# Kernel optimization log

Hardware: AMD Instinct MI355X
Metric: run time of the kernel (lower is better)

The kernel has to match this reference:

```python
import jax, jax.numpy as jnp
import numpy as np

N = 50000          # nodes (cells)
G = 1000           # input genes
E = 800000         # edges
HIDDEN = 128
HEADS = 8
C_HID = HIDDEN // HEADS   # 16 per-head channels
LATENT = 16
NEG_SLOPE = 0.2


def _gat_layer(x, src, dst, W, a_src, a_dst, b, heads, out_ch, concat):
    """PyG GATConv (shared lin for src/dst, add_self_loops=False, eval mode)."""
    n = x.shape[0]
    h = (x @ W).reshape(n, heads, out_ch)                 # [N,H,C]
    al_s = jnp.einsum('nhc,hc->nh', h, a_src)             # [N,H]
    al_d = jnp.einsum('nhc,hc->nh', h, a_dst)             # [N,H]
    logits = jax.nn.leaky_relu(al_s[src] + al_d[dst], NEG_SLOPE)  # [E,H]
    # segment softmax over destination neighborhoods
    m = jax.ops.segment_max(logits, dst, num_segments=n)  # [N,H]
    m = jnp.where(jnp.isfinite(m), m, 0.0)                # empty segments -> 0
    e = jnp.exp(logits - m[dst])                          # [E,H]
    denom = jax.ops.segment_sum(e, dst, num_segments=n)   # [N,H]
    alpha = e / (denom[dst] + 1e-16)                      # [E,H]
    msg = h[src] * alpha[:, :, None]                      # [E,H,C]
    out = jax.ops.segment_sum(msg, dst, num_segments=n)   # [N,H,C]
    out = out.reshape(n, heads * out_ch) if concat else out.mean(axis=1)
    return out + b


def setup_inputs() -> dict:
    key = jax.random.key(0)
    ks = jax.random.split(key, 16)
    x = jax.random.normal(ks[0], (N, G), dtype=jnp.float32)
    edge_index = jax.random.randint(ks[1], (2, E), 0, N, dtype=jnp.int64)

    def glorot(k, shape):
        fan_in, fan_out = shape[0], shape[-1]
        s = jnp.sqrt(6.0 / (fan_in + fan_out)).astype(jnp.float32)
        return jax.random.uniform(k, shape, jnp.float32, -s, s)

    # layer 0: G -> 8 heads x 16 (concat -> 128)
    W0 = glorot(ks[2], (G, HEADS * C_HID))
    as0 = glorot(ks[3], (HEADS, C_HID))
    ad0 = glorot(ks[4], (HEADS, C_HID))
    b0 = jnp.zeros((HEADS * C_HID,), jnp.float32)
    # layer 1: 128 -> 8 heads x 16 (concat -> 128)
    W1 = glorot(ks[5], (HIDDEN, HEADS * C_HID))
    as1 = glorot(ks[6], (HEADS, C_HID))
    ad1 = glorot(ks[7], (HEADS, C_HID))
    b1 = jnp.zeros((HEADS * C_HID,), jnp.float32)
    # layer 2: 128 -> 1 head x 16 (concat=False -> 16)
    W2 = glorot(ks[8], (HIDDEN, LATENT))
    as2 = glorot(ks[9], (1, LATENT))
    ad2 = glorot(ks[10], (1, LATENT))
    b2 = jnp.zeros((LATENT,), jnp.float32)

    return {"x": x, "edge_index": edge_index,
            "W0": W0, "as0": as0, "ad0": ad0, "b0": b0,
            "W1": W1, "as1": as1, "ad1": ad1, "b1": b1,
            "W2": W2, "as2": as2, "ad2": ad2, "b2": b2}


def reference(x, edge_index, W0, as0, ad0, b0, W1, as1, ad1, b1, W2, as2, ad2, b2):
    src, dst = edge_index[0], edge_index[1]
    h = _gat_layer(x, src, dst, W0, as0, ad0, b0, HEADS, C_HID, concat=True)
    h = jax.nn.elu(h)
    h = _gat_layer(h, src, dst, W1, as1, ad1, b1, HEADS, C_HID, concat=True)
    h = jax.nn.elu(h)
    z = _gat_layer(h, src, dst, W2, as2, ad2, b2, 1, LATENT, concat=False)
    return z
```

## Files before the change

### kernel.cpp

```cpp
#include <hip/hip_runtime.h>
#include <hip/hip_bf16.h>
#include <math.h>

#define GENES 1000

typedef __attribute__((ext_vector_type(8))) _Float16 half8;
typedef __attribute__((ext_vector_type(4))) float f32x4;
typedef __attribute__((ext_vector_type(4))) unsigned int uint4v;
typedef __attribute__((ext_vector_type(2))) unsigned int uint2v;

__device__ inline float f16lo(unsigned int v) {
  return (float)__builtin_bit_cast(_Float16, (unsigned short)(v & 0xffffu));
}
__device__ inline float f16hi(unsigned int v) {
  return (float)__builtin_bit_cast(_Float16, (unsigned short)(v >> 16));
}


__global__ void k_deg(const int* __restrict__ ei, int* __restrict__ deg, int E) {
  int e = blockIdx.x * blockDim.x + threadIdx.x;
  if (e < E) atomicAdd(&deg[ei[E + e]], 1);
}

__global__ void k_scan1(const int* __restrict__ deg, int* __restrict__ ptr,
                        int* __restrict__ bsum, int n) {
  __shared__ int ws[4];
  int t = threadIdx.x, b = blockIdx.x;
  int i = b * 256 + t;
  int lane = t & 63, w = t >> 6;
  int x = (i < n) ? deg[i] : 0;
  #pragma unroll
  for (int d = 1; d < 64; d <<= 1) {
    int y = __shfl_up(x, d);
    if (lane >= d) x += y;
  }
  if (lane == 63) ws[w] = x;
  __syncthreads();
  if (t == 0) {
    int s = 0;
    #pragma unroll
    for (int k = 0; k < 4; ++k) { s += ws[k]; ws[k] = s; }
  }
  __syncthreads();
  int incl = x + (w ? ws[w - 1] : 0);
  if (i < n) ptr[i + 1] = incl;
  if (t == 255) bsum[b] = incl;
  if (i == 0) ptr[0] = 0;
}

__global__ void k_scan2(int* __restrict__ bsum, int nb) {
  __shared__ int ws[4];
  int t = threadIdx.x;
  int lane = t & 63, w = t >> 6;
  int v = (t < nb) ? bsum[t] : 0;
  int x = v;
  #pragma unroll
  for (int d = 1; d < 64; d <<= 1) {
    int y = __shfl_up(x, d);
    if (lane >= d) x += y;
  }
  if (lane == 63) ws[w] = x;
  __syncthreads();
  if (t == 0) {
    int s = 0;
    #pragma unroll
    for (int k = 0; k < 4; ++k) { s += ws[k]; ws[k] = s; }
  }
  __syncthreads();
  int incl = x + (w ? ws[w - 1] : 0);
  if (t < nb) bsum[t] = incl - v;
}

__global__ void k_scan3(int* __restrict__ ptr, const int* __restrict__ bsum, int n) {
  int i = blockIdx.x * 256 + threadIdx.x;
  if (i < n) ptr[i + 1] += bsum[blockIdx.x];
}

__global__ void k_scatter(const int* __restrict__ ei, const int* __restrict__ ptr,
                          int* __restrict__ cur, int* __restrict__ srcs, int E) {
  int e = blockIdx.x * blockDim.x + threadIdx.x;
  if (e >= E) return;
  int d = ei[E + e];
  int pos = ptr[d] + atomicAdd(&cur[d], 1);
  srcs[pos] = ei[e];
}


__global__ void k_wpackall(const float* __restrict__ W0, const float* __restrict__ W1,
                           const float* __restrict__ W2, unsigned short* __restrict__ P,
                           int K0) {
  int t = blockIdx.x * blockDim.x + threadIdx.x;
  if (t >= 163840) return;
  const float* W; int K, N, e;
  if (t < 131072)      { W = W0; K = K0;  N = 128; e = t; }
  else if (t < 147456) { W = W1; K = 128; N = 128; e = t - 131072; }
  else                 { W = W2; K = 128; N = 16;  e = t - 147456; }
  int s = e >> 12, rem = e & 4095;
  int q = rem >> 10, col = (rem >> 3) & 127, j = rem & 7;
  int k = s * 32 + q * 8 + j;
  float v = (k < K && col < N) ? W[(long)k * N + col] : 0.f;
  _Float16 h = (_Float16)v;
  P[t] = __builtin_bit_cast(unsigned short, h);
}


template<int HH, bool AF16, bool OF16>
__global__ __launch_bounds__(512) void k_mgemm7(
    const void* __restrict__ Ap, const unsigned short* __restrict__ Pb,
    void* __restrict__ outp, float* __restrict__ als, float* __restrict__ ald,
    const float* __restrict__ avs, const float* __restrict__ avd,
    int M, int K, int nst, int ldc) {
  __shared__ __align__(16) char lds[24576];
  char* bA0 = lds;
  char* bA1 = lds + 4096;
  char* bB0 = lds + 8192;
  char* bB1 = lds + 16384;

  int t = threadIdx.x, lane = t & 63;
  int r15 = lane & 15, q = lane >> 4;
  int wv = t >> 6;
  int wr = wv >> 1, wc = wv & 1;
  long row0 = (long)blockIdx.x * 64;

  int srow = t >> 3, sseg = t & 7;
  long arow = row0 + srow; if (arow >= M) arow = M - 1;
  const float* pa32 = (const float*)Ap + arow * (long)K;
  const unsigned short* pa16 = (const unsigned short*)Ap + arow * (long)K;

  f32x4 acc[4];
  #pragma unroll
  for (int nt = 0; nt < 4; ++nt) acc[nt] = (f32x4){0.f, 0.f, 0.f, 0.f};

  uint4v rA0, rA1, rB0, rB1;
  uint2v sA0, sA1;

  auto loadA = [&](int s, uint4v& r32, uint2v& r16) {
    int k0 = s * 32 + sseg * 4;
    if constexpr (AF16) {
      r16 = (k0 < K) ? *(const uint2v*)(pa16 + k0) : (uint2v){0u, 0u};
    } else {
      r32 = (k0 < K) ? *(const uint4v*)(pa32 + k0) : (uint4v){0u, 0u, 0u, 0u};
    }
  };
  auto writeA = [&](char* buf, uint4v r32, uint2v r16) {
    char* p = buf + ((sseg >> 1) * 1024 + srow * 16 + (sseg & 1) * 8);
    if constexpr (AF16) {
      *(uint2v*)p = r16;
    } else {
      float4 f = __builtin_bit_cast(float4, r32);
      uint2v h;
      h[0] = __builtin_bit_cast(unsigned int, __builtin_amdgcn_cvt_pkrtz(f.x, f.y));
      h[1] = __builtin_bit_cast(unsigned int, __builtin_amdgcn_cvt_pkrtz(f.z, f.w));
      *(uint2v*)p = h;
    }
  };
  auto loadB = [&](int s, uint4v& r) {
    r = *(const uint4v*)(Pb + (size_t)s * 4096 + t * 8);
  };
  auto writeB = [&](char* buf, uint4v r) {
    *(uint4v*)(buf + t * 16) = r;
  };
  auto compute = [&](const char* bA, const char* bB) {
    half8 af = *(const half8*)(bA + q * 1024 + (wr * 16 + r15) * 16);
    #pragma unroll
    for (int nt = 0; nt < 4; ++nt) {
      half8 bf = *(const half8*)(bB + q * 2048 + (wc * 64 + nt * 16 + r15) * 16);
      acc[nt] = __builtin_amdgcn_mfma_f32_16x16x32_f16(af, bf, acc[nt], 0, 0, 0);
    }
  };

  loadA(0, rA0, sA0); loadB(0, rB0);
  if (nst > 1) { loadA(1, rA1, sA1); loadB(1, rB1); }
  writeA(bA0, rA0, sA0); writeB(bB0, rB0);
  __syncthreads();

  for (int s = 0; s < nst; s += 2) {
    if (s + 2 < nst) { loadA(s + 2, rA0, sA0); loadB(s + 2, rB0); }
    compute(bA0, bB0);
    if (s + 1 < nst) { writeA(bA1, rA1, sA1); writeB(bB1, rB1); }
    __syncthreads();
    if (s + 1 < nst) {
      if (s + 3 < nst) { loadA(s + 3, rA1, sA1); loadB(s + 3, rB1); }
      compute(bA1, bB1);
      if (s + 2 < nst) { writeA(bA0, rA0, sA0); writeB(bB0, rB0); }
      __syncthreads();
    }
  }

  long rbase = row0 + wr * 16 + q * 4;
  if constexpr (OF16) {
    unsigned short* o16 = (unsigned short*)outp;
    #pragma unroll
    for (int i = 0; i < 4; ++i) {
      long r = rbase + i;
      if (r < M) {
        #pragma unroll
        for (int nt = 0; nt < 4; ++nt) {
          int col = wc * 64 + nt * 16 + r15;
          _Float16 hv = (_Float16)acc[nt][i];
          o16[r * ldc + col] = __builtin_bit_cast(unsigned short, hv);
        }
      }
    }
  } else {
    float* o32 = (float*)outp;
    #pragma unroll
    for (int i = 0; i < 4; ++i) {
      long r = rbase + i;
      if (r < M) {
        #pragma unroll
        for (int nt = 0; nt < 4; ++nt) {
          int col = wc * 64 + nt * 16 + r15;
          if (col < ldc) o32[r * ldc + col] = acc[nt][i];
        }
      }
    }
  }
  #pragma unroll
  for (int nt = 0; nt < 4; ++nt) {
    int head = wc * 4 + nt;
    if (head < HH) {
      float cs = avs[head * 16 + r15];
      float cd = avd[head * 16 + r15];
      #pragma unroll
      for (int i = 0; i < 4; ++i) {
        float s1 = acc[nt][i] * cs;
        float s2 = acc[nt][i] * cd;
        #pragma unroll
        for (int d = 1; d < 16; d <<= 1) {
          s1 += __shfl_xor(s1, d);
          s2 += __shfl_xor(s2, d);
        }
        if (r15 == 0) {
          long r = rbase + i;
          if (r < M) { als[r * HH + head] = s1; ald[r * HH + head] = s2; }
        }
      }
    }
  }
}


__global__ void k_agg128h(const unsigned short* __restrict__ h,
                          const float* __restrict__ als, const float* __restrict__ ald,
                          const int* __restrict__ ptr, const int* __restrict__ srcs,
                          const float* __restrict__ bias,
                          unsigned short* __restrict__ out, int n) {
  int wid = (int)(((long)blockIdx.x * blockDim.x + threadIdx.x) >> 6);
  if (wid >= n) return;
  int lane = threadIdx.x & 63;
  int half = lane >> 5, l5 = lane & 31;
  int c0 = 4 * l5;
  int hB = l5 >> 2;
  int p0 = ptr[wid], deg = ptr[wid + 1] - p0;
  float aldB = ald[wid * 8 + hB];
  float a0 = 0.f, a1 = 0.f, a2 = 0.f, a3 = 0.f, dsum = 0.f;
  int j = half;
  for (; j + 6 < deg; j += 8) {
    int s0 = srcs[p0 + j],     s1 = srcs[p0 + j + 2];
    int s2 = srcs[p0 + j + 4], s3 = srcs[p0 + j + 6];
    float l0 = als[s0 * 8 + hB] + aldB;
    float l1 = als[s1 * 8 + hB] + aldB;
    float l2 = als[s2 * 8 + hB] + aldB;
    float l3 = als[s3 * 8 + hB] + aldB;
    uint2v h0 = *(const uint2v*)(h + (long)s0 * 128 + c0);
    uint2v h1 = *(const uint2v*)(h + (long)s1 * 128 + c0);
    uint2v h2 = *(const uint2v*)(h + (long)s2 * 128 + c0);
    uint2v h3 = *(const uint2v*)(h + (long)s3 * 128 + c0);
    l0 = l0 > 0.f ? l0 : 0.2f * l0;
    l1 = l1 > 0.f ? l1 : 0.2f * l1;
    l2 = l2 > 0.f ? l2 : 0.2f * l2;
    l3 = l3 > 0.f ? l3 : 0.2f * l3;
    float e0 = __expf(l0), e1 = __expf(l1), e2 = __expf(l2), e3 = __expf(l3);
    dsum += e0 + e1 + e2 + e3;
    a0 += e0 * f16lo(h0[0]) + e1 * f16lo(h1[0]) + e2 * f16lo(h2[0]) + e3 * f16lo(h3[0]);
    a1 += e0 * f16hi(h0[0]) + e1 * f16hi(h1[0]) + e2 * f16hi(h2[0]) + e3 * f16hi(h3[0]);
    a2 += e0 * f16lo(h0[1]) + e1 * f16lo(h1[1]) + e2 * f16lo(h2[1]) + e3 * f16lo(h3[1]);
    a3 += e0 * f16hi(h0[1]) + e1 * f16hi(h1[1]) + e2 * f16hi(h2[1]) + e3 * f16hi(h3[1]);
  }
  for (; j < deg; j += 2) {
    int s = srcs[p0 + j];
    float l = als[s * 8 + hB] + aldB;
    l = l > 0.f ? l : 0.2f * l;
    float e = __expf(l);
    uint2v hv = *(const uint2v*)(h + (long)s * 128 + c0);
    dsum += e;
    a0 += e * f16lo(hv[0]);
    a1 += e * f16hi(hv[0]);
    a2 += e * f16lo(hv[1]);
    a3 += e * f16hi(hv[1]);
  }
  a0 += __shfl_xor(a0, 32);
  a1 += __shfl_xor(a1, 32);
  a2 += __shfl_xor(a2, 32);
  a3 += __shfl_xor(a3, 32);
  dsum += __shfl_xor(dsum, 32);
  if (half == 0) {
    float inv = 1.f / (dsum + 1e-16f);
    float o0 = a0 * inv + bias[c0];
    float o1 = a1 * inv + bias[c0 + 1];
    float o2 = a2 * inv + bias[c0 + 2];
    float o3 = a3 * inv + bias[c0 + 3];
    o0 = o0 > 0.f ? o0 : (__expf(o0) - 1.f);
    o1 = o1 > 0.f ? o1 : (__expf(o1) - 1.f);
    o2 = o2 > 0.f ? o2 : (__expf(o2) - 1.f);
    o3 = o3 > 0.f ? o3 : (__expf(o3) - 1.f);
    uint2v po;
    po[0] = __builtin_bit_cast(unsigned int, __builtin_amdgcn_cvt_pkrtz(o0, o1));
    po[1] = __builtin_bit_cast(unsigned int, __builtin_amdgcn_cvt_pkrtz(o2, o3));
    *(uint2v*)(out + (long)wid * 128 + c0) = po;
  }
}


__global__ void k_agg16(const float* __restrict__ h, const float* __restrict__ als,
                        const float* __restrict__ ald, const int* __restrict__ ptr,
                        const int* __restrict__ srcs, const float* __restrict__ bias,
                        float* __restrict__ out, int n, int lda) {
  int wid = (int)(((long)blockIdx.x * blockDim.x + threadIdx.x) >> 6);
  if (wid >= n) return;
  int lane = threadIdx.x & 63;
  int p0 = ptr[wid], deg = ptr[wid + 1] - p0;
  float aldv = ald[wid];
  int g = lane >> 4, c = lane & 15;
  float acc = 0.f, dsum = 0.f;
  int j = g;
  for (; j + 12 < deg; j += 16) {
    int s0 = srcs[p0 + j],     s1 = srcs[p0 + j + 4];
    int s2 = srcs[p0 + j + 8], s3 = srcs[p0 + j + 12];
    float l0 = als[s0] + aldv, l1 = als[s1] + aldv;
    float l2 = als[s2] + aldv, l3 = als[s3] + aldv;
    float h0 = h[(long)s0 * lda + c], h1 = h[(long)s1 * lda + c];
    float h2 = h[(long)s2 * lda + c], h3 = h[(long)s3 * lda + c];
    l0 = l0 > 0.f ? l0 : 0.2f * l0;
    l1 = l1 > 0.f ? l1 : 0.2f * l1;
    l2 = l2 > 0.f ? l2 : 0.2f * l2;
    l3 = l3 > 0.f ? l3 : 0.2f * l3;
    float e0 = __expf(l0), e1 = __expf(l1), e2 = __expf(l2), e3 = __expf(l3);
    dsum += e0 + e1 + e2 + e3;
    acc += e0 * h0 + e1 * h1 + e2 * h2 + e3 * h3;
  }
  for (; j < deg; j += 4) {
    int s = srcs[p0 + j];
    float l = als[s] + aldv;
    l = l > 0.f ? l : 0.2f * l;
    float e = __expf(l);
    dsum += e;
    acc += e * h[(long)s * lda + c];
  }
  #pragma unroll
  for (int d = 16; d < 64; d <<= 1) {
    acc += __shfl_xor(acc, d);
    dsum += __shfl_xor(dsum, d);
  }
  if (lane < 16)
    out[(long)wid * 16 + lane] = acc / (dsum + 1e-16f) + bias[lane];
}


extern "C" void kernel_launch(void* const* d_in, const int* in_sizes, int n_in,
                              void* d_out, int out_size, void* d_ws, size_t ws_size,
                              hipStream_t stream) {
  const float* x  = (const float*)d_in[0];
  const int*   ei = (const int*)d_in[1];
  const float* W0 = (const float*)d_in[2];
  const float* as0= (const float*)d_in[3];
  const float* ad0= (const float*)d_in[4];
  const float* b0 = (const float*)d_in[5];
  const float* W1 = (const float*)d_in[6];
  const float* as1= (const float*)d_in[7];
  const float* ad1= (const float*)d_in[8];
  const float* b1 = (const float*)d_in[9];
  const float* W2 = (const float*)d_in[10];
  const float* as2= (const float*)d_in[11];
  const float* ad2= (const float*)d_in[12];
  const float* b2 = (const float*)d_in[13];
  float* out = (float*)d_out;

  int E = in_sizes[1] / 2;
  int n = in_sizes[0] / GENES;

  char* ws = (char*)d_ws;
  size_t off = 0;
  auto alloc = [&](size_t bytes) {
    void* p = ws + off;
    off = (off + bytes + 255) & ~(size_t)255;
    return p;
  };
  int* ptr   = (int*)alloc((size_t)(n + 1) * sizeof(int));
  int* cur   = (int*)alloc((size_t)n * sizeof(int));
  int* bsum  = (int*)alloc(512 * sizeof(int));
  int* srcs  = (int*)alloc((size_t)E * sizeof(int));
  unsigned short* Ah = (unsigned short*)alloc((size_t)n * 128 * sizeof(unsigned short));
  unsigned short* Bh = (unsigned short*)alloc((size_t)n * 128 * sizeof(unsigned short));
  float* A2  = (float*)alloc((size_t)n * 16 * sizeof(float));
  float* als = (float*)alloc((size_t)n * 8 * sizeof(float));
  float* ald = (float*)alloc((size_t)n * 8 * sizeof(float));
  unsigned short* P = (unsigned short*)alloc((size_t)163840 * sizeof(unsigned short));
  unsigned short* P0 = P;
  unsigned short* P1 = P + 131072;
  unsigned short* P2 = P + 147456;

  int eb = (E + 255) / 256;
  int nb = (n + 255) / 256;
  hipMemsetAsync(cur, 0, (size_t)n * sizeof(int), stream);
  k_deg<<<eb, 256, 0, stream>>>(ei, cur, E);
  k_scan1<<<nb, 256, 0, stream>>>(cur, ptr, bsum, n);
  k_scan2<<<1, 256, 0, stream>>>(bsum, nb);
  k_scan3<<<nb, 256, 0, stream>>>(ptr, bsum, n);
  hipMemsetAsync(cur, 0, (size_t)n * sizeof(int), stream);
  k_scatter<<<eb, 256, 0, stream>>>(ei, ptr, cur, srcs, E);
  k_wpackall<<<640, 256, 0, stream>>>(W0, W1, W2, P, GENES);

  int mgb  = (n + 63) / 64;
  int aggb = (int)(((long)n * 64 + 255) / 256);

  k_mgemm7<8, false, true><<<mgb, 512, 0, stream>>>(
      x, P0, Ah, als, ald, as0, ad0, n, GENES, 32, 128);
  k_agg128h<<<aggb, 256, 0, stream>>>(Ah, als, ald, ptr, srcs, b0, Bh, n);

  k_mgemm7<8, true, true><<<mgb, 512, 0, stream>>>(
      Bh, P1, Ah, als, ald, as1, ad1, n, 128, 4, 128);
  k_agg128h<<<aggb, 256, 0, stream>>>(Ah, als, ald, ptr, srcs, b1, Bh, n);

  k_mgemm7<1, true, false><<<mgb, 512, 0, stream>>>(
      Bh, P2, A2, als, ald, as2, ad2, n, 128, 4, 16);
  k_agg16<<<aggb, 256, 0, stream>>>(A2, als, ald, ptr, srcs, b2, out, n, 16);
}
```

Measured before the change: 275.1 us.

## Deepen A-tile prefetch to three stages and make GEMM stage count a template

Measured after the change: 275.8 us. Within noise of the previous version (+0.2%).

```diff
diff --git a/kernel.cpp b/kernel.cpp
--- a/kernel.cpp
+++ b/kernel.cpp
@@ -22,13 +22,14 @@
   if (e < E) atomicAdd(&deg[ei[E + e]], 1);
 }
 
-__global__ void k_scan1(const int* __restrict__ deg, int* __restrict__ ptr,
+__global__ void k_scan1(int* __restrict__ deg, int* __restrict__ ptr,
                         int* __restrict__ bsum, int n) {
   __shared__ int ws[4];
   int t = threadIdx.x, b = blockIdx.x;
   int i = b * 256 + t;
   int lane = t & 63, w = t >> 6;
-  int x = (i < n) ? deg[i] : 0;
+  int x = 0;
+  if (i < n) { x = deg[i]; deg[i] = 0; }
   #pragma unroll
   for (int d = 1; d < 64; d <<= 1) {
     int y = __shfl_up(x, d);
@@ -104,12 +105,12 @@
 }
 
 
-template<int HH, bool AF16, bool OF16>
-__global__ __launch_bounds__(512) void k_mgemm7(
+template<int HH, int NST, bool AF16, bool OF16>
+__global__ __launch_bounds__(512) void k_mgemm8(
     const void* __restrict__ Ap, const unsigned short* __restrict__ Pb,
     void* __restrict__ outp, float* __restrict__ als, float* __restrict__ ald,
     const float* __restrict__ avs, const float* __restrict__ avd,
-    int M, int K, int nst, int ldc) {
+    int M, int K, int ldc) {
   __shared__ __align__(16) char lds[24576];
   char* bA0 = lds;
   char* bA1 = lds + 4096;
@@ -131,8 +132,9 @@
   #pragma unroll
   for (int nt = 0; nt < 4; ++nt) acc[nt] = (f32x4){0.f, 0.f, 0.f, 0.f};
 
-  uint4v rA0, rA1, rB0, rB1;
-  uint2v sA0, sA1;
+  uint4v aA0, aA1, aA2;
+  uint2v aH0, aH1, aH2;
+  uint4v rB0, rB1;
 
   auto loadA = [&](int s, uint4v& r32, uint2v& r16) {
     int k0 = s * 32 + sseg * 4;
@@ -154,6 +156,18 @@
       *(uint2v*)p = h;
     }
   };
+  auto ldA3 = [&](int tile) {
+    int sl = tile % 3;
+    if (sl == 0) loadA(tile, aA0, aH0);
+    else if (sl == 1) loadA(tile, aA1, aH1);
+    else loadA(tile, aA2, aH2);
+  };
+  auto wrA3 = [&](char* buf, int tile) {
+    int sl = tile % 3;
+    if (sl == 0) writeA(buf, aA0, aH0);
+    else if (sl == 1) writeA(buf, aA1, aH1);
+    else writeA(buf, aA2, aH2);
+  };
   auto loadB = [&](int s, uint4v& r) {
     r = *(const uint4v*)(Pb + (size_t)s * 4096 + t * 8);
   };
@@ -169,20 +183,24 @@
     }
   };
 
-  loadA(0, rA0, sA0); loadB(0, rB0);
-  if (nst > 1) { loadA(1, rA1, sA1); loadB(1, rB1); }
-  writeA(bA0, rA0, sA0); writeB(bB0, rB0);
+  ldA3(0); loadB(0, rB0);
+  ldA3(1); loadB(1, rB1);
+  ldA3(2);
+  wrA3(bA0, 0); writeB(bB0, rB0);
   __syncthreads();
 
-  for (int s = 0; s < nst; s += 2) {
-    if (s + 2 < nst) { loadA(s + 2, rA0, sA0); loadB(s + 2, rB0); }
+  #pragma unroll
+  for (int s = 0; s < NST; s += 2) {
+    if (s + 3 < NST) ldA3(s + 3);
+    if (s + 2 < NST) loadB(s + 2, rB0);
     compute(bA0, bB0);
-    if (s + 1 < nst) { writeA(bA1, rA1, sA1); writeB(bB1, rB1); }
+    if (s + 1 < NST) { wrA3(bA1, s + 1); writeB(bB1, rB1); }
     __syncthreads();
-    if (s + 1 < nst) {
-      if (s + 3 < nst) { loadA(s + 3, rA1, sA1); loadB(s + 3, rB1); }
+    if (s + 1 < NST) {
+      if (s + 4 < NST) ldA3(s + 4);
+      if (s + 3 < NST) loadB(s + 3, rB1);
       compute(bA1, bB1);
-      if (s + 2 < nst) { writeA(bA0, rA0, sA0); writeB(bB0, rB0); }
+      if (s + 2 < NST) { wrA3(bA0, s + 2); writeB(bB0, rB0); }
       __syncthreads();
     }
   }
@@ -408,22 +426,21 @@
   k_scan1<<<nb, 256, 0, stream>>>(cur, ptr, bsum, n);
   k_scan2<<<1, 256, 0, stream>>>(bsum, nb);
   k_scan3<<<nb, 256, 0, stream>>>(ptr, bsum, n);
-  hipMemsetAsync(cur, 0, (size_t)n * sizeof(int), stream);
   k_scatter<<<eb, 256, 0, stream>>>(ei, ptr, cur, srcs, E);
   k_wpackall<<<640, 256, 0, stream>>>(W0, W1, W2, P, GENES);
 
   int mgb  = (n + 63) / 64;
   int aggb = (int)(((long)n * 64 + 255) / 256);
 
-  k_mgemm7<8, false, true><<<mgb, 512, 0, stream>>>(
-      x, P0, Ah, als, ald, as0, ad0, n, GENES, 32, 128);
+  k_mgemm8<8, 32, false, true><<<mgb, 512, 0, stream>>>(
+      x, P0, Ah, als, ald, as0, ad0, n, GENES, 128);
   k_agg128h<<<aggb, 256, 0, stream>>>(Ah, als, ald, ptr, srcs, b0, Bh, n);
 
-  k_mgemm7<8, true, true><<<mgb, 512, 0, stream>>>(
-      Bh, P1, Ah, als, ald, as1, ad1, n, 128, 4, 128);
+  k_mgemm8<8, 4, true, true><<<mgb, 512, 0, stream>>>(
+      Bh, P1, Ah, als, ald, as1, ad1, n, 128, 128);
   k_agg128h<<<aggb, 256, 0, stream>>>(Ah, als, ald, ptr, srcs, b1, Bh, n);
 
-  k_mgemm7<1, true, false><<<mgb, 512, 0, stream>>>(
-      Bh, P2, A2, als, ald, as2, ad2, n, 128, 4, 16);
+  k_mgemm8<1, 4, true, false><<<mgb, 512, 0, stream>>>(
+      Bh, P2, A2, als, ald, as2, ad2, n, 128, 16);
   k_agg16<<<aggb, 256, 0, stream>>>(A2, als, ald, ptr, srcs, b2, out, n, 16);
 }
```

## Widen GEMM K-chunk to 128 with padded LDS, drop second memset

Applied to the files above, without the earlier changes.

Measured after the change: 274.3 us. No clear change (-0.3%).

```diff
diff --git a/kernel.cpp b/kernel.cpp
--- a/kernel.cpp
+++ b/kernel.cpp
@@ -15,6 +15,9 @@
 __device__ inline float f16hi(unsigned int v) {
   return (float)__builtin_bit_cast(_Float16, (unsigned short)(v >> 16));
 }
+__device__ inline unsigned int pk(float a, float b) {
+  return __builtin_bit_cast(unsigned int, __builtin_amdgcn_cvt_pkrtz(a, b));
+}
 
 
 __global__ void k_deg(const int* __restrict__ ei, int* __restrict__ deg, int E) {
@@ -22,13 +25,14 @@
   if (e < E) atomicAdd(&deg[ei[E + e]], 1);
 }
 
-__global__ void k_scan1(const int* __restrict__ deg, int* __restrict__ ptr,
+__global__ void k_scan1(int* __restrict__ deg, int* __restrict__ ptr,
                         int* __restrict__ bsum, int n) {
   __shared__ int ws[4];
   int t = threadIdx.x, b = blockIdx.x;
   int i = b * 256 + t;
   int lane = t & 63, w = t >> 6;
-  int x = (i < n) ? deg[i] : 0;
+  int x = 0;
+  if (i < n) { x = deg[i]; deg[i] = 0; }
   #pragma unroll
   for (int d = 1; d < 64; d <<= 1) {
     int y = __shfl_up(x, d);
@@ -95,9 +99,9 @@
   if (t < 131072)      { W = W0; K = K0;  N = 128; e = t; }
   else if (t < 147456) { W = W1; K = 128; N = 128; e = t - 131072; }
   else                 { W = W2; K = 128; N = 16;  e = t - 147456; }
-  int s = e >> 12, rem = e & 4095;
-  int q = rem >> 10, col = (rem >> 3) & 127, j = rem & 7;
-  int k = s * 32 + q * 8 + j;
+  int c = e >> 14, ks = (e >> 12) & 3, q = (e >> 10) & 3;
+  int col = (e >> 3) & 127, j = e & 7;
+  int k = c * 128 + ks * 32 + q * 8 + j;
   float v = (k < K && col < N) ? W[(long)k * N + col] : 0.f;
   _Float16 h = (_Float16)v;
   P[t] = __builtin_bit_cast(unsigned short, h);
@@ -105,16 +109,14 @@
 
 
 template<int HH, bool AF16, bool OF16>
-__global__ __launch_bounds__(512) void k_mgemm7(
+__global__ __launch_bounds__(512) void k_mgemm9(
     const void* __restrict__ Ap, const unsigned short* __restrict__ Pb,
     void* __restrict__ outp, float* __restrict__ als, float* __restrict__ ald,
     const float* __restrict__ avs, const float* __restrict__ avd,
-    int M, int K, int nst, int ldc) {
-  __shared__ __align__(16) char lds[24576];
-  char* bA0 = lds;
-  char* bA1 = lds + 4096;
-  char* bB0 = lds + 8192;
-  char* bB1 = lds + 16384;
+    int M, int K, int nmac, int ldc) {
+  __shared__ __align__(16) char lds[16640 + 32768];
+  char* As = lds;
+  char* Bs = lds + 16640;
 
   int t = threadIdx.x, lane = t & 63;
   int r15 = lane & 15, q = lane >> 4;
@@ -122,68 +124,96 @@
   int wr = wv >> 1, wc = wv & 1;
   long row0 = (long)blockIdx.x * 64;
 
-  int srow = t >> 3, sseg = t & 7;
+  int srow = t >> 3, seg = t & 7;
   long arow = row0 + srow; if (arow >= M) arow = M - 1;
   const float* pa32 = (const float*)Ap + arow * (long)K;
   const unsigned short* pa16 = (const unsigned short*)Ap + arow * (long)K;
+  int aks = seg >> 1, aq0 = (seg & 1) * 2;
+  char* wA0 = As + aks * 4160 + aq0 * 1040 + srow * 16;
+  char* wA1 = wA0 + 1040;
+  const char* pbB = (const char*)Pb;
 
   f32x4 acc[4];
   #pragma unroll
   for (int nt = 0; nt < 4; ++nt) acc[nt] = (f32x4){0.f, 0.f, 0.f, 0.f};
 
-  uint4v rA0, rA1, rB0, rB1;
-  uint2v sA0, sA1;
-
-  auto loadA = [&](int s, uint4v& r32, uint2v& r16) {
-    int k0 = s * 32 + sseg * 4;
+  uint4v a0, a1, a2, a3;
+  uint4v b0, b1, b2, b3;
+
+  auto issueA = [&](int c) {
+    int k0 = c * 128 + seg * 16;
     if constexpr (AF16) {
-      r16 = (k0 < K) ? *(const uint2v*)(pa16 + k0) : (uint2v){0u, 0u};
+      uint4v z = (uint4v){0u,0u,0u,0u};
+      a0 = (k0 + 8 <= K)  ? *(const uint4v*)(pa16 + k0)     : z;
+      a1 = (k0 + 16 <= K) ? *(const uint4v*)(pa16 + k0 + 8) : z;
     } else {
-      r32 = (k0 < K) ? *(const uint4v*)(pa32 + k0) : (uint4v){0u, 0u, 0u, 0u};
+      if (k0 + 16 <= K) {
+        a0 = *(const uint4v*)(pa32 + k0);
+        a1 = *(const uint4v*)(pa32 + k0 + 4);
+        a2 = *(const uint4v*)(pa32 + k0 + 8);
+        a3 = *(const uint4v*)(pa32 + k0 + 12);
+      } else {
+        float tmp[16];
+        #pragma unroll
+        for (int ii = 0; ii < 16; ++ii)
+          tmp[ii] = (k0 + ii < K) ? pa32[k0 + ii] : 0.f;
+        a0 = __builtin_bit_cast(uint4v, make_float4(tmp[0], tmp[1], tmp[2], tmp[3]));
+        a1 = __builtin_bit_cast(uint4v, make_float4(tmp[4], tmp[5], tmp[6], tmp[7]));
+        a2 = __builtin_bit_cast(uint4v, make_float4(tmp[8], tmp[9], tmp[10], tmp[11]));
+        a3 = __builtin_bit_cast(uint4v, make_float4(tmp[12], tmp[13], tmp[14], tmp[15]));
+      }
     }
   };
-  auto writeA = [&](char* buf, uint4v r32, uint2v r16) {
-    char* p = buf + ((sseg >> 1) * 1024 + srow * 16 + (sseg & 1) * 8);
+  auto issueB = [&](int c) {
+    const char* p = pbB + (size_t)c * 32768 + t * 16;
+    b0 = *(const uint4v*)(p);
+    b1 = *(const uint4v*)(p + 8192);
+    b2 = *(const uint4v*)(p + 16384);
+    b3 = *(const uint4v*)(p + 24576);
+  };
+  auto writeA = [&]() {
     if constexpr (AF16) {
-      *(uint2v*)p = r16;
+      *(uint4v*)wA0 = a0;
+      *(uint4v*)wA1 = a1;
     } else {
-      float4 f = __builtin_bit_cast(float4, r32);
-      uint2v h;
-      h[0] = __builtin_bit_cast(unsigned int, __builtin_amdgcn_cvt_pkrtz(f.x, f.y));
-      h[1] = __builtin_bit_cast(unsigned int, __builtin_amdgcn_cvt_pkrtz(f.z, f.w));
-      *(uint2v*)p = h;
+      float4 f0 = __builtin_bit_cast(float4, a0);
+      float4 f1 = __builtin_bit_cast(float4, a1);
+      float4 f2 = __builtin_bit_cast(float4, a2);
+      float4 f3 = __builtin_bit_cast(float4, a3);
+      uint4v h0, h1;
+      h0[0] = pk(f0.x, f0.y); h0[1] = pk(f0.z, f0.w);
+      h0[2] = pk(f1.x, f1.y); h0[3] = pk(f1.z, f1.w);
+      h1[0] = pk(f2.x, f2.y); h1[1] = pk(f2.z, f2.w);
+      h1[2] = pk(f3.x, f3.y); h1[3] = pk(f3.z, f3.w);
+      *(uint4v*)wA0 = h0;
+      *(uint4v*)wA1 = h1;
     }
   };
-  auto loadB = [&](int s, uint4v& r) {
-    r = *(const uint4v*)(Pb + (size_t)s * 4096 + t * 8);
+  auto writeB = [&]() {
+    char* p = Bs + t * 16;
+    *(uint4v*)(p)         = b0;
+    *(uint4v*)(p + 8192)  = b1;
+    *(uint4v*)(p + 16384) = b2;
+    *(uint4v*)(p + 24576) = b3;
   };
-  auto writeB = [&](char* buf, uint4v r) {
-    *(uint4v*)(buf + t * 16) = r;
-  };
-  auto compute = [&](const char* bA, const char* bB) {
-    half8 af = *(const half8*)(bA + q * 1024 + (wr * 16 + r15) * 16);
+
+  issueA(0); issueB(0);
+
+  for (int c = 0; c < nmac; ++c) {
+    __syncthreads();
+    writeA();
+    writeB();
+    __syncthreads();
+    if (c + 1 < nmac) { issueA(c + 1); issueB(c + 1); }
     #pragma unroll
-    for (int nt = 0; nt < 4; ++nt) {
-      half8 bf = *(const half8*)(bB + q * 2048 + (wc * 64 + nt * 16 + r15) * 16);
-      acc[nt] = __builtin_amdgcn_mfma_f32_16x16x32_f16(af, bf, acc[nt], 0, 0, 0);
-    }
-  };
-
-  loadA(0, rA0, sA0); loadB(0, rB0);
-  if (nst > 1) { loadA(1, rA1, sA1); loadB(1, rB1); }
-  writeA(bA0, rA0, sA0); writeB(bB0, rB0);
-  __syncthreads();
-
-  for (int s = 0; s < nst; s += 2) {
-    if (s + 2 < nst) { loadA(s + 2, rA0, sA0); loadB(s + 2, rB0); }
-    compute(bA0, bB0);
-    if (s + 1 < nst) { writeA(bA1, rA1, sA1); writeB(bB1, rB1); }
-    __syncthreads();
-    if (s + 1 < nst) {
-      if (s + 3 < nst) { loadA(s + 3, rA1, sA1); loadB(s + 3, rB1); }
-      compute(bA1, bB1);
-      if (s + 2 < nst) { writeA(bA0, rA0, sA0); writeB(bB0, rB0); }
-      __syncthreads();
+    for (int ks2 = 0; ks2 < 4; ++ks2) {
+      half8 af = *(const half8*)(As + ks2 * 4160 + q * 1040 + (wr * 16 + r15) * 16);
+      #pragma unroll
+      for (int nt = 0; nt < 4; ++nt) {
+        half8 bf = *(const half8*)(Bs + ks2 * 8192 + q * 2048 +
+                                   (wc * 64 + nt * 16 + r15) * 16);
+        acc[nt] = __builtin_amdgcn_mfma_f32_16x16x32_f16(af, bf, acc[nt], 0, 0, 0);
+      }
     }
   }
 
@@ -408,22 +438,21 @@
   k_scan1<<<nb, 256, 0, stream>>>(cur, ptr, bsum, n);
   k_scan2<<<1, 256, 0, stream>>>(bsum, nb);
   k_scan3<<<nb, 256, 0, stream>>>(ptr, bsum, n);
-  hipMemsetAsync(cur, 0, (size_t)n * sizeof(int), stream);
   k_scatter<<<eb, 256, 0, stream>>>(ei, ptr, cur, srcs, E);
   k_wpackall<<<640, 256, 0, stream>>>(W0, W1, W2, P, GENES);
 
   int mgb  = (n + 63) / 64;
   int aggb = (int)(((long)n * 64 + 255) / 256);
 
-  k_mgemm7<8, false, true><<<mgb, 512, 0, stream>>>(
-      x, P0, Ah, als, ald, as0, ad0, n, GENES, 32, 128);
+  k_mgemm9<8, false, true><<<mgb, 512, 0, stream>>>(
+      x, P0, Ah, als, ald, as0, ad0, n, GENES, 8, 128);
   k_agg128h<<<aggb, 256, 0, stream>>>(Ah, als, ald, ptr, srcs, b0, Bh, n);
 
-  k_mgemm7<8, true, true><<<mgb, 512, 0, stream>>>(
-      Bh, P1, Ah, als, ald, as1, ad1, n, 128, 4, 128);
+  k_mgemm9<8, true, true><<<mgb, 512, 0, stream>>>(
+      Bh, P1, Ah, als, ald, as1, ad1, n, 128, 1, 128);
   k_agg128h<<<aggb, 256, 0, stream>>>(Ah, als, ald, ptr, srcs, b1, Bh, n);
 
-  k_mgemm7<1, true, false><<<mgb, 512, 0, stream>>>(
-      Bh, P2, A2, als, ald, as2, ad2, n, 128, 4, 16);
+  k_mgemm9<1, true, false><<<mgb, 512, 0, stream>>>(
+      Bh, P2, A2, als, ald, as2, ad2, n, 128, 1, 16);
   k_agg16<<<aggb, 256, 0, stream>>>(A2, als, ald, ptr, srcs, b2, out, n, 16);
 }
```

## Stream layer-0 fp32 activations directly to LDS with swizzled layout

Applied to the files above, without the earlier changes.

Result: no change. 273.4 us (-0.6%).

```diff
diff --git a/kernel.cpp b/kernel.cpp
--- a/kernel.cpp
+++ b/kernel.cpp
@@ -15,6 +15,15 @@
 __device__ inline float f16hi(unsigned int v) {
   return (float)__builtin_bit_cast(_Float16, (unsigned short)(v >> 16));
 }
+__device__ inline unsigned int pk(float a, float b) {
+  return __builtin_bit_cast(unsigned int, __builtin_amdgcn_cvt_pkrtz(a, b));
+}
+
+__device__ inline void gload16(const void* g, void* l) {
+  __builtin_amdgcn_global_load_lds(
+      (const __attribute__((address_space(1))) unsigned int*)g,
+      (__attribute__((address_space(3))) unsigned int*)l, 16, 0, 0);
+}
 
 
 __global__ void k_deg(const int* __restrict__ ei, int* __restrict__ deg, int E) {
@@ -22,13 +31,14 @@
   if (e < E) atomicAdd(&deg[ei[E + e]], 1);
 }
 
-__global__ void k_scan1(const int* __restrict__ deg, int* __restrict__ ptr,
+__global__ void k_scan1(int* __restrict__ deg, int* __restrict__ ptr,
                         int* __restrict__ bsum, int n) {
   __shared__ int ws[4];
   int t = threadIdx.x, b = blockIdx.x;
   int i = b * 256 + t;
   int lane = t & 63, w = t >> 6;
-  int x = (i < n) ? deg[i] : 0;
+  int x = 0;
+  if (i < n) { x = deg[i]; deg[i] = 0; }
   #pragma unroll
   for (int d = 1; d < 64; d <<= 1) {
     int y = __shfl_up(x, d);
@@ -104,6 +114,99 @@
 }
 
 
+__global__ __launch_bounds__(512) void k_mgemm11(
+    const float* __restrict__ A, const unsigned short* __restrict__ Pb,
+    unsigned short* __restrict__ outp, float* __restrict__ als,
+    float* __restrict__ ald, const float* __restrict__ avs,
+    const float* __restrict__ avd, int M, int K) {
+  __shared__ __align__(16) char lds[32768];
+
+  int t = threadIdx.x, lane = t & 63, wv = t >> 6;
+  int r15 = lane & 15, q = lane >> 4;
+  int wr = wv >> 1, wc = wv & 1;
+  long row0 = (long)blockIdx.x * 64;
+
+  int srow = wv * 8 + (lane >> 3);
+  int sseg = lane & 7;
+  int gseg = sseg ^ (srow & 7);
+  long arow = row0 + srow; if (arow >= M) arow = M - 1;
+  const char* gA = (const char*)(A + arow * (long)K) + gseg * 16;
+  const char* gB = (const char*)Pb + t * 16;
+
+  f32x4 acc[4];
+  #pragma unroll
+  for (int nt = 0; nt < 4; ++nt) acc[nt] = (f32x4){0.f, 0.f, 0.f, 0.f};
+
+  auto issue = [&](int s) {
+    char* Ab = lds + (s & 1) * 8192;
+    char* Bb = lds + 16384 + (s & 1) * 8192;
+    gload16(gA + (size_t)s * 128, Ab + t * 16);
+    gload16(gB + (size_t)s * 8192, Bb + t * 16);
+  };
+  auto compute = [&](int s) {
+    const char* Ab = lds + (s & 1) * 8192;
+    const char* Bb = lds + 16384 + (s & 1) * 8192;
+    int row = wr * 16 + r15;
+    int sw = row & 7;
+    uint4v alo = *(const uint4v*)(Ab + row * 128 + ((2 * q) ^ sw) * 16);
+    uint4v ahi = *(const uint4v*)(Ab + row * 128 + ((2 * q + 1) ^ sw) * 16);
+    float4 lo = __builtin_bit_cast(float4, alo);
+    float4 hi = __builtin_bit_cast(float4, ahi);
+    uint4v au;
+    au[0] = pk(lo.x, lo.y); au[1] = pk(lo.z, lo.w);
+    au[2] = pk(hi.x, hi.y); au[3] = pk(hi.z, hi.w);
+    half8 af = __builtin_bit_cast(half8, au);
+    #pragma unroll
+    for (int nt = 0; nt < 4; ++nt) {
+      half8 bf = *(const half8*)(Bb + q * 2048 + (wc * 64 + nt * 16 + r15) * 16);
+      acc[nt] = __builtin_amdgcn_mfma_f32_16x16x32_f16(af, bf, acc[nt], 0, 0, 0);
+    }
+  };
+
+  issue(0);
+  __syncthreads();
+  for (int s = 0; s < 32; ++s) {
+    if (s + 1 < 32) issue(s + 1);
+    compute(s);
+    __syncthreads();
+  }
+
+  long rbase = row0 + wr * 16 + q * 4;
+  #pragma unroll
+  for (int i = 0; i < 4; ++i) {
+    long r = rbase + i;
+    if (r < M) {
+      #pragma unroll
+      for (int nt = 0; nt < 4; ++nt) {
+        int col = wc * 64 + nt * 16 + r15;
+        _Float16 hv = (_Float16)acc[nt][i];
+        outp[r * 128 + col] = __builtin_bit_cast(unsigned short, hv);
+      }
+    }
+  }
+  #pragma unroll
+  for (int nt = 0; nt < 4; ++nt) {
+    int head = wc * 4 + nt;
+    float cs = avs[head * 16 + r15];
+    float cd = avd[head * 16 + r15];
+    #pragma unroll
+    for (int i = 0; i < 4; ++i) {
+      float s1 = acc[nt][i] * cs;
+      float s2 = acc[nt][i] * cd;
+      #pragma unroll
+      for (int d = 1; d < 16; d <<= 1) {
+        s1 += __shfl_xor(s1, d);
+        s2 += __shfl_xor(s2, d);
+      }
+      if (r15 == 0) {
+        long r = rbase + i;
+        if (r < M) { als[r * 8 + head] = s1; ald[r * 8 + head] = s2; }
+      }
+    }
+  }
+}
+
+
 template<int HH, bool AF16, bool OF16>
 __global__ __launch_bounds__(512) void k_mgemm7(
     const void* __restrict__ Ap, const unsigned short* __restrict__ Pb,
@@ -149,8 +252,8 @@
     } else {
       float4 f = __builtin_bit_cast(float4, r32);
       uint2v h;
-      h[0] = __builtin_bit_cast(unsigned int, __builtin_amdgcn_cvt_pkrtz(f.x, f.y));
-      h[1] = __builtin_bit_cast(unsigned int, __builtin_amdgcn_cvt_pkrtz(f.z, f.w));
+      h[0] = pk(f.x, f.y);
+      h[1] = pk(f.z, f.w);
       *(uint2v*)p = h;
     }
   };
@@ -408,15 +511,13 @@
   k_scan1<<<nb, 256, 0, stream>>>(cur, ptr, bsum, n);
   k_scan2<<<1, 256, 0, stream>>>(bsum, nb);
   k_scan3<<<nb, 256, 0, stream>>>(ptr, bsum, n);
-  hipMemsetAsync(cur, 0, (size_t)n * sizeof(int), stream);
   k_scatter<<<eb, 256, 0, stream>>>(ei, ptr, cur, srcs, E);
   k_wpackall<<<640, 256, 0, stream>>>(W0, W1, W2, P, GENES);
 
   int mgb  = (n + 63) / 64;
   int aggb = (int)(((long)n * 64 + 255) / 256);
 
-  k_mgemm7<8, false, true><<<mgb, 512, 0, stream>>>(
-      x, P0, Ah, als, ald, as0, ad0, n, GENES, 32, 128);
+  k_mgemm11<<<mgb, 512, 0, stream>>>(x, P0, Ah, als, ald, as0, ad0, n, GENES);
   k_agg128h<<<aggb, 256, 0, stream>>>(Ah, als, ald, ptr, srcs, b0, Bh, n);
 
   k_mgemm7<8, true, true><<<mgb, 512, 0, stream>>>(
```
